# Optimization experiments

Measured on AMD Instinct MI355X. Metric: run time of the kernel, lower is better.

## Reference

```python
import jax, jax.numpy as jnp
import numpy as np

K = 9                # snake kernel size
CENTER = K // 2
EXT = 1.0            # extend_scope
EPS = 1e-5           # GroupNorm eps (torch default)


def conv2d(x, w, b, stride, padding):
    out = jax.lax.conv_general_dilated(
        x, w, window_strides=stride, padding=padding,
        dimension_numbers=("NCHW", "OIHW", "NCHW"))
    return out + b[None, :, None, None]


def group_norm(x, gamma, beta, groups):
    B, C, H, W = x.shape
    xg = x.reshape(B, groups, C // groups, H, W)
    mu = xg.mean(axis=(2, 3, 4), keepdims=True)
    var = xg.var(axis=(2, 3, 4), keepdims=True)
    xn = ((xg - mu) / jnp.sqrt(var + EPS)).reshape(B, C, H, W)
    return xn * gamma[None, :, None, None] + beta[None, :, None, None]


def setup_inputs() -> dict:
    key = jax.random.key(0)
    ks = jax.random.split(key, 6)
    B, Cin, Cout, H, W = 4, 64, 64, 128, 128
    x = jax.random.normal(ks[0], (B, Cin, H, W), jnp.float32)
    w_off = jax.random.normal(ks[1], (2 * K, Cin, 3, 3), jnp.float32) * 0.05
    b_off = jax.random.normal(ks[2], (2 * K,), jnp.float32) * 0.01
    g_gn_off = jnp.ones((2 * K,), jnp.float32)
    b_gn_off = jnp.zeros((2 * K,), jnp.float32)
    w_dsc = jax.random.normal(ks[3], (Cout, Cin, K, 1), jnp.float32) * 0.05
    b_dsc = jax.random.normal(ks[4], (Cout,), jnp.float32) * 0.01
    g_gn = jnp.ones((Cout,), jnp.float32)
    b_gn = jnp.zeros((Cout,), jnp.float32)
    return {"x": x, "w_off": w_off, "b_off": b_off,
            "g_gn_off": g_gn_off, "b_gn_off": b_gn_off,
            "w_dsc": w_dsc, "b_dsc": b_dsc, "g_gn": g_gn, "b_gn": b_gn}


def reference(x, w_off, b_off, g_gn_off, b_gn_off, w_dsc, b_dsc, g_gn, b_gn):
    B, Cin, H, W = x.shape
    # offset branch: conv3x3 -> GN(K groups over 2K chans) -> tanh
    off = conv2d(x, w_off, b_off, (1, 1), "SAME")
    off = jnp.tanh(group_norm(off, g_gn_off, b_gn_off, K))
    y_off = off[:, :K]                              # morph=0 uses y offsets, [B,K,H,W]

    # cumulative offsets outward from the kernel center (center entry = 0)
    upper = jnp.cumsum(y_off[:, CENTER + 1:], axis=1)
    lower = jnp.flip(jnp.cumsum(jnp.flip(y_off[:, :CENTER], axis=1), axis=1), axis=1)
    y_off_new = jnp.concatenate(
        [lower, jnp.zeros_like(y_off[:, :1]), upper], axis=1)   # [B,K,H,W]

    # coordinate maps (pixel space)
    y_coord = jnp.arange(H, dtype=x.dtype)[None, None, :, None] + EXT * y_off_new
    x_spread = jnp.linspace(-CENTER, CENTER, K).astype(x.dtype)
    x_coord = jnp.broadcast_to(
        jnp.arange(W, dtype=x.dtype)[None, None, None, :]
        + x_spread[None, :, None, None], y_coord.shape)
    # rearrange b k h w -> b (h k) w
    y_map = y_coord.transpose(0, 2, 1, 3).reshape(B, H * K, W)
    x_map = x_coord.transpose(0, 2, 1, 3).reshape(B, H * K, W)

    # bilinear grid_sample, align_corners=True; clamp-to-range == torch's
    # _coordinate_map_scaling(clamp + [-1,1] normalize) then grid_sample
    yc = jnp.clip(y_map, 0.0, H - 1.0)
    xc = jnp.clip(x_map, 0.0, W - 1.0)
    y0 = jnp.floor(yc); x0 = jnp.floor(xc)
    wy = yc - y0; wx = xc - x0
    y0i = y0.astype(jnp.int32); x0i = x0.astype(jnp.int32)
    y1i = jnp.minimum(y0i + 1, H - 1); x1i = jnp.minimum(x0i + 1, W - 1)

    def samp(f, y0i, y1i, x0i, x1i, wy, wx):
        # f: [C,H,W]; indices/weights: [K*H, W] -> [C, K*H, W]
        v00 = f[:, y0i, x0i]; v01 = f[:, y0i, x1i]
        v10 = f[:, y1i, x0i]; v11 = f[:, y1i, x1i]
        return (v00 * (1 - wy) * (1 - wx) + v01 * (1 - wy) * wx
                + v10 * wy * (1 - wx) + v11 * wy * wx)

    deformed = jax.vmap(samp)(x, y0i, y1i, x0i, x1i, wy, wx)  # [B,C,K*H,W]

    # snake conv: kernel (K,1), stride (K,1), then GN(out//4) + ReLU
    out = conv2d(deformed, w_dsc, b_dsc, (K, 1), "VALID")      # [B,Cout,H,W]
    out = group_norm(out, g_gn, b_gn, w_dsc.shape[0] // 4)
    return jax.nn.relu(out)
```

## Files before the change

kernel.cpp:

```cpp
#include <hip/hip_runtime.h>
#include <hip/hip_bf16.h>
#include <math.h>

#define B 4
#define C 64
#define H 128
#define W 128
#define KK 9
#define CENTER 4
#define HW (H*W)
#define HP 130
#define WP 130

typedef __attribute__((ext_vector_type(8))) short short8;
typedef __attribute__((ext_vector_type(4))) float f4;

#define OFF_OFFT   0
#define OFF_XB     786432
#define OFF_WB     2949632
#define OFF_WOB    2968064
#define OFF_CSUM   2972672
#define OFF_OSUM   2980864

__device__ __forceinline__ unsigned bf16pack(float a, float b) {
    unsigned ua = __builtin_bit_cast(unsigned, a) + 0x8000u;
    unsigned ub = __builtin_bit_cast(unsigned, b) + 0x8000u;
    return __builtin_amdgcn_perm(ub, ua, 0x07060302);
}

__device__ __forceinline__ unsigned lerp_pack(unsigned a, unsigned b, float fw) {
    float alo = __builtin_bit_cast(float, a << 16);
    float ahi = __builtin_bit_cast(float, a & 0xffff0000u);
    float blo = __builtin_bit_cast(float, b << 16);
    float bhi = __builtin_bit_cast(float, b & 0xffff0000u);
    float slo = alo + fw * (blo - alo);
    float shi = ahi + fw * (bhi - ahi);
    return bf16pack(slo, shi);
}

__device__ __forceinline__ float fast_tanh(float x) {
    float e = __expf(2.f * x);
    return 1.f - 2.f * __builtin_amdgcn_rcpf(e + 1.f);
}

__global__ __launch_bounds__(256) void k_prep(const float* __restrict__ x,
                                              const float* __restrict__ w_dsc,
                                              const float* __restrict__ w_off,
                                              unsigned short* __restrict__ xb,
                                              unsigned short* __restrict__ wb,
                                              unsigned short* __restrict__ wob,
                                              float* __restrict__ csum) {
    int bid = blockIdx.x;
    int tid = threadIdx.x;
    if (bid < 2048) {
        __shared__ float lt[64 * 33];
        int xcd = bid & 7, i = bid >> 3;
        int c = i & 3, hc = (i >> 2) & 15, b = i >> 6;
        int h = (xcd << 4) | hc;
        int w0 = c * 32;
        int ciA = tid >> 2, gA = tid & 3;
        int wlB = tid >> 3, cgB = tid & 7;

        if (c == 0 && tid < 8)
            *(uint4*)(xb + ((size_t)(b * HP + h + 1) * WP) * 64 + tid * 8)
                = make_uint4(0, 0, 0, 0);
        if (c == 3 && tid < 8)
            *(uint4*)(xb + (((size_t)(b * HP + h + 1) * WP) + WP - 1) * 64 + tid * 8)
                = make_uint4(0, 0, 0, 0);
        {
            const float* src = x + ((size_t)(b * C + ciA) * HW) + h * W + w0 + gA * 8;
            float4 v0 = *(const float4*)src;
            float4 v1 = *(const float4*)(src + 4);
            float* d = lt + ciA * 33 + gA * 8;
            d[0] = v0.x; d[1] = v0.y; d[2] = v0.z; d[3] = v0.w;
            d[4] = v1.x; d[5] = v1.y; d[6] = v1.z; d[7] = v1.w;
        }
        __syncthreads();
        {
            unsigned u[4];
#pragma unroll
            for (int i2 = 0; i2 < 4; i2++) {
                float lo = lt[(cgB * 8 + 2 * i2)     * 33 + wlB];
                float hi = lt[(cgB * 8 + 2 * i2 + 1) * 33 + wlB];
                u[i2] = bf16pack(lo, hi);
            }
            *(uint4*)(xb + ((size_t)((b * HP + h + 1) * WP + w0 + wlB + 1)) * 64 + cgB * 8) =
                make_uint4(u[0], u[1], u[2], u[3]);
        }
    } else if (bid < 2048 + 8) {
        int r = bid - 2048;
        int b = r >> 1, which = r & 1;
        unsigned short* dst = xb + ((size_t)(b * HP + which * (HP - 1)) * WP) * 64;
        for (int t = tid; t < WP * 64 / 8; t += 256)
            *(uint4*)(dst + t * 8) = make_uint4(0, 0, 0, 0);
    } else if (bid < 2048 + 8 + 180) {
        int idx = (bid - (2048 + 8)) * 256 + tid;
        if (idx < KK * C * C) {
            int k  = idx >> 12;
            int r  = idx & 4095;
            int co = r >> 6;
            int ci = r & 63;
            unsigned u = __builtin_bit_cast(unsigned, w_dsc[(co * C + ci) * KK + k]);
            u = (u + 0x7fffu + ((u >> 16) & 1u)) >> 16;
            wb[idx] = (unsigned short)u;
        } else if (idx < KK * C * C + 9 * 16 * 64) {
            int r   = idx - KK * C * C;
            int tap = r >> 10;
            int j   = (r >> 6) & 15;
            int ci  = r & 63;
            float v = (j < 10) ? w_off[(j * C + ci) * 9 + tap] : 0.f;
            unsigned u = __builtin_bit_cast(unsigned, v);
            u = (u + 0x7fffu + ((u >> 16) & 1u)) >> 16;
            wob[r] = (unsigned short)u;
        }
    } else {
        int z = bid - (2048 + 8 + 180);
        int base = z * 1024 + tid * 4;
        *(f4*)(csum + base) = 0;
    }
}

__global__ __launch_bounds__(256, 4) void k_offconv(const unsigned short* __restrict__ xb,
                                                    const unsigned short* __restrict__ wob,
                                                    const float* __restrict__ b_off,
                                                    float* __restrict__ offT,
                                                    float* __restrict__ osum16) {
    __shared__ unsigned short wlds[1152 * 8];
    __shared__ float red[80];
    int bid = blockIdx.x;
    int xcd  = bid & 7;
    int i    = bid >> 3;
    int b    = i >> 5;
    int rest = i & 31;
    int h    = (xcd << 4) | (rest >> 1);
    int half = rest & 1;
    int tid  = threadIdx.x;
    int wid  = tid >> 6;
    int lane = tid & 63;
    int lm = lane & 15, qd = lane >> 4;
    int pw = half * 64 + wid * 16;

    for (int c = tid; c < 1152; c += 256) {
        int row = c >> 3, g = c & 7;
        uint4 v = *(const uint4*)(wob + c * 8);
        int dst = (g ^ (row & 7)) * 144 + row;
        *(uint4*)(wlds + dst * 8) = v;
    }
    __syncthreads();

    f4 acc = 0;
    const unsigned short* xrow = xb + ((size_t)(b * HP + h) * WP) * 64;
#pragma unroll
    for (int s = 0; s < 2; s++) {
        int co_ofs = s * 32 + qd * 8;
        short8 a_[9];
#pragma unroll
        for (int t = 0; t < 9; t++) {
            int ky = t / 3, kx = t - 3 * (t / 3);
            a_[t] = *(const short8*)(xrow +
                ((size_t)(ky * WP + pw + lm + kx)) * 64 + co_ofs);
        }
#pragma unroll
        for (int t = 0; t < 9; t++) {
            int row = t * 16 + lm;
            int chunk = (((s * 4 + qd) ^ (lm & 7)) * 144) + row;
            short8 w = *(const short8*)(wlds + chunk * 8);
            acc = __builtin_amdgcn_mfma_f32_16x16x32_bf16(a_[t], w, acc, 0, 0, 0);
        }
    }

    float bo = b_off[lm];
    float sv = 0.f, sq = 0.f;
    int pixbase = (b * H + h) * W;
#pragma unroll
    for (int r = 0; r < 4; r++) {
        float val = acc[r] + bo;
        int p = pw + qd * 4 + r;
        if (lm < 10) {
            offT[(size_t)(pixbase + p) * 12 + lm] = val;
            sv += val; sq += val * val;
        }
    }
    sv += __shfl_xor(sv, 16); sv += __shfl_xor(sv, 32);
    sq += __shfl_xor(sq, 16); sq += __shfl_xor(sq, 32);
    if (lane < 16 && lm < 10) {
        red[(wid * 10 + lm) * 2]     = sv;
        red[(wid * 10 + lm) * 2 + 1] = sq;
    }
    __syncthreads();
    if (tid < 20) {
        int j = tid >> 1, comp = tid & 1;
        float s = red[j * 2 + comp] + red[(10 + j) * 2 + comp] +
                  red[(20 + j) * 2 + comp] + red[(30 + j) * 2 + comp];
        int sidx = (h >> 3) & 15;
        atomicAdd(&osum16[sidx * 40 + b * 10 + (j >> 1) * 2 + comp], s);
    }
}

__global__ __launch_bounds__(256, 4) void k_main(const unsigned short* __restrict__ xb,
                                                 const float* __restrict__ offT,
                                                 const float* __restrict__ osum16,
                                                 const float* __restrict__ g_gn_off,
                                                 const float* __restrict__ b_gn_off,
                                                 const unsigned short* __restrict__ wb,
                                                 const float* __restrict__ b_dsc,
                                                 float* __restrict__ outp,
                                                 float* __restrict__ csum16) {
    __shared__ unsigned short wlds[2304 * 8];
    __shared__ float red[512];
    __shared__ float sred[16];

    int bid = blockIdx.x;
    int xcd  = bid & 7;
    int i    = bid >> 3;
    int b    = i >> 5;
    int rest = i & 31;
    int h    = (xcd << 4) | (rest >> 1);
    int p0   = (rest & 1) << 6;
    int tid  = threadIdx.x;
    int wid  = tid >> 6;
    int lane = tid & 63;
    int lm = lane & 15, qd = lane >> 4;

    int ps = p0 + wid * 16 + lm;

    if (tid < 160) {
        int gc = tid >> 4, s = tid & 15;
        float v = osum16[s * 40 + b * 10 + gc];
        v += __shfl_xor(v, 1); v += __shfl_xor(v, 2);
        v += __shfl_xor(v, 4); v += __shfl_xor(v, 8);
        if (s == 0) sred[gc] = v;
    }
    for (int c = tid; c < 2304; c += 256) {
        int k = c >> 8, row = (c >> 2) & 63, g2 = c & 3;
        uint4 v = *(const uint4*)(wb + (size_t)k * 4096 + row * 64 + g2 * 8);
        int dst = ((g2 ^ (row & 3)) * 576) + k * 64 + row;
        *(uint4*)(wlds + dst * 8) = v;
    }
    __syncthreads();

    float yoff[KK];
    {
        const float inv_n = 1.f / (2.f * HW);
        const float* op = offT + (size_t)((b * H + h) * W + ps) * 12;
        f4 o0 = *(const f4*)op;
        f4 o1 = *(const f4*)(op + 4);
        float o8 = op[8];
        float raw[KK] = {o0[0], o0[1], o0[2], o0[3], o1[0], o1[1], o1[2], o1[3], o8};
        float v[KK];
#pragma unroll
        for (int j = 0; j < KK; j++) {
            int g = j >> 1;
            float s  = sred[g * 2];
            float s2 = sred[g * 2 + 1];
            float mean = s * inv_n;
            float var  = s2 * inv_n - mean * mean;
            float rstd = rsqrtf(var + 1e-5f);
            v[j] = fast_tanh((raw[j] - mean) * rstd * g_gn_off[j] + b_gn_off[j]);
        }
        yoff[CENTER] = 0.f;
        float run = 0.f;
#pragma unroll
        for (int k = CENTER - 1; k >= 0; k--) { run += v[k]; yoff[k] = run; }
        run = 0.f;
#pragma unroll
        for (int k = CENTER + 1; k < KK; k++) { run += v[k]; yoff[k] = run; }
    }

    f4 acc[4];
#pragma unroll
    for (int ct = 0; ct < 4; ct++) acc[ct] = 0;

    auto kpass = [&](int s) {
        int so = s * 32;
#pragma unroll
        for (int kg = 0; kg < 3; kg++) {
            int   ofsA[3], ofsB[3];
            float fw[3];
#pragma unroll
            for (int j = 0; j < 3; j++) {
                int k = kg * 3 + j;
                float yc = fminf(fmaxf((float)h + yoff[k], 0.f), (float)(H - 1));
                float fy = floorf(yc);
                int y0 = (int)fy;
                int dy = (y0 < H - 1) ? (WP * 64) : 0;
                fw[j] = yc - fy;
                int xi = min(max(ps + k - CENTER, 0), W - 1);
                ofsA[j] = ((b * HP + y0 + 1) * WP + xi + 1) * 64 + qd * 8 + so;
                ofsB[j] = ofsA[j] + dy;
            }
            uint4 ga[3], gb[3];
#pragma unroll
            for (int j = 0; j < 3; j++) {
                ga[j] = *(const uint4*)(xb + ofsA[j]);
                gb[j] = *(const uint4*)(xb + ofsB[j]);
            }
#pragma unroll
            for (int j = 0; j < 3; j++) {
                int k = kg * 3 + j;
                uint4 r;
                r.x = lerp_pack(ga[j].x, gb[j].x, fw[j]);
                r.y = lerp_pack(ga[j].y, gb[j].y, fw[j]);
                r.z = lerp_pack(ga[j].z, gb[j].z, fw[j]);
                r.w = lerp_pack(ga[j].w, gb[j].w, fw[j]);
                short8 afr = __builtin_bit_cast(short8, r);
#pragma unroll
                for (int ct = 0; ct < 4; ct++) {
                    int row = ct * 16 + lm;
                    int chunk = ((qd ^ (lm & 3)) * 576) + k * 64 + row;
                    short8 bfr = *(const short8*)(wlds + chunk * 8);
                    acc[ct] = __builtin_amdgcn_mfma_f32_16x16x32_bf16(afr, bfr,
                                                                      acc[ct], 0, 0, 0);
                }
            }
        }
    };

    kpass(0);
    __syncthreads();
    for (int c = tid; c < 2304; c += 256) {
        int k = c >> 8, row = (c >> 2) & 63, g2 = c & 3;
        uint4 v = *(const uint4*)(wb + (size_t)k * 4096 + row * 64 + (4 + g2) * 8);
        int dst = ((g2 ^ (row & 3)) * 576) + k * 64 + row;
        *(uint4*)(wlds + dst * 8) = v;
    }
    __syncthreads();
    kpass(1);

#pragma unroll
    for (int ct = 0; ct < 4; ct++) {
        int co = ct * 16 + lm;
        float bias = b_dsc[co];
        f4 v;
        float sv = 0.f, sq = 0.f;
#pragma unroll
        for (int r = 0; r < 4; r++) {
            v[r] = acc[ct][r] + bias;
            sv += v[r]; sq += v[r] * v[r];
        }
        *(f4*)(outp + ((size_t)(b * C + co)) * HW + h * W + p0 + wid * 16 + qd * 4) = v;
        sv += __shfl_xor(sv, 16); sv += __shfl_xor(sv, 32);
        sq += __shfl_xor(sq, 16); sq += __shfl_xor(sq, 32);
        if (lane < 16) {
            red[((wid * 4 + ct) * 16 + lm) * 2]     = sv;
            red[((wid * 4 + ct) * 16 + lm) * 2 + 1] = sq;
        }
    }
    __syncthreads();
    if (tid < 128) {
        int co = tid >> 1, comp = tid & 1;
        int ct = co >> 4, lmr = co & 15;
        float s = 0.f;
#pragma unroll
        for (int w2 = 0; w2 < 4; w2++)
            s += red[((w2 * 4 + ct) * 16 + lmr) * 2 + comp];
        int sidx = (h >> 3) & 15;
        atomicAdd(&csum16[(sidx * 256 + b * 64 + co) * 2 + comp], s);
    }
}

__global__ __launch_bounds__(256) void k_norm(float* __restrict__ outp,
                                              const float* __restrict__ csum16,
                                              const float* __restrict__ g_gn,
                                              const float* __restrict__ b_gn) {
    __shared__ float lds[128];
    int bid = blockIdx.x;
    int xcd = bid & 7;
    int i   = bid >> 3;
    int bc  = i >> 1;
    int c2  = (xcd << 1) | (i & 1);
    int b = bc >> 6, co = bc & 63;
    int grp = co >> 2;
    int tid = threadIdx.x;

    if (tid < 128) {
        int s = tid >> 3, c = (tid >> 1) & 3, comp = tid & 1;
        lds[tid] = csum16[(s * 256 + b * 64 + grp * 4 + c) * 2 + comp];
    }
    __syncthreads();
#pragma unroll
    for (int st = 64; st >= 2; st >>= 1) {
        if (tid < st) lds[tid] += lds[tid + st];
        __syncthreads();
    }
    float S = lds[0], S2 = lds[1];
    float n = 4.f * HW;
    float mean = S / n;
    float var  = S2 / n - mean * mean;
    float rstd = rsqrtf(var + 1e-5f);
    float sc = rstd * g_gn[co];
    float sh = b_gn[co] - mean * sc;

    int idx = (bc * 16 + c2) * 256 + tid;
    float4* ptr = (float4*)outp;
    float4 vv = ptr[idx];
    vv.x = fmaxf(vv.x * sc + sh, 0.f);
    vv.y = fmaxf(vv.y * sc + sh, 0.f);
    vv.z = fmaxf(vv.z * sc + sh, 0.f);
    vv.w = fmaxf(vv.w * sc + sh, 0.f);
    ptr[idx] = vv;
}

extern "C" void kernel_launch(void* const* d_in, const int* in_sizes, int n_in,
                              void* d_out, int out_size, void* d_ws, size_t ws_size,
                              hipStream_t stream) {
    const float* x        = (const float*)d_in[0];
    const float* w_off    = (const float*)d_in[1];
    const float* b_off    = (const float*)d_in[2];
    const float* g_gn_off = (const float*)d_in[3];
    const float* b_gn_off = (const float*)d_in[4];
    const float* w_dsc    = (const float*)d_in[5];
    const float* b_dsc    = (const float*)d_in[6];
    const float* g_gn     = (const float*)d_in[7];
    const float* b_gn     = (const float*)d_in[8];
    float* out = (float*)d_out;
    float* ws  = (float*)d_ws;

    float*          offT   = ws + OFF_OFFT;
    unsigned short* xbp    = (unsigned short*)(ws + OFF_XB);
    unsigned short* wbp    = (unsigned short*)(ws + OFF_WB);
    unsigned short* wobp   = (unsigned short*)(ws + OFF_WOB);
    float*          csum16 = ws + OFF_CSUM;
    float*          osum16 = ws + OFF_OSUM;

    k_prep<<<2048 + 8 + 180 + 9, 256, 0, stream>>>(x, w_dsc, w_off, xbp, wbp,
                                                   wobp, csum16);
    k_offconv<<<2 * B * H, 256, 0, stream>>>(xbp, wobp, b_off, offT, osum16);
    k_main<<<2 * B * H, 256, 0, stream>>>(xbp, offT, osum16, g_gn_off, b_gn_off,
                                          wbp, b_dsc, out, csum16);
    k_norm<<<B * C * HW / 4 / 256, 256, 0, stream>>>(out, csum16, g_gn, b_gn);
}
```

Measured before the change: 134.9 us.

## Process full row per 512-thread block with whole weight tensor resident in LDS

k_main now uses 512-thread blocks that each cover a full output row of 128 pixels, halving the grid. The whole bf16 snake-conv weight (both channel halves) is staged into LDS once, which removes the mid-kernel barrier and reload between the two channel passes. Gathers for both channel halves are issued together per kernel group to raise memory-level parallelism. The cost is doubled LDS per block (about 74KB), larger blocks, and higher register pressure, all of which can lower occupancy.

New measurement: 137.3 us. About the same (+1.8%).

```diff
diff --git a/kernel.cpp b/kernel.cpp
--- a/kernel.cpp
+++ b/kernel.cpp
@@ -197,7 +197,7 @@
     }
 }
 
-__global__ __launch_bounds__(256, 4) void k_main(const unsigned short* __restrict__ xb,
+__global__ __launch_bounds__(512, 4) void k_main(const unsigned short* __restrict__ xb,
                                                  const float* __restrict__ offT,
                                                  const float* __restrict__ osum16,
                                                  const float* __restrict__ g_gn_off,
@@ -206,23 +206,21 @@
                                                  const float* __restrict__ b_dsc,
                                                  float* __restrict__ outp,
                                                  float* __restrict__ csum16) {
-    __shared__ unsigned short wlds[2304 * 8];
-    __shared__ float red[512];
+    __shared__ unsigned short wlds[4608 * 8];
+    __shared__ float red[1024];
     __shared__ float sred[16];
 
     int bid = blockIdx.x;
     int xcd  = bid & 7;
     int i    = bid >> 3;
-    int b    = i >> 5;
-    int rest = i & 31;
-    int h    = (xcd << 4) | (rest >> 1);
-    int p0   = (rest & 1) << 6;
+    int b    = i >> 4;
+    int h    = (xcd << 4) | (i & 15);
     int tid  = threadIdx.x;
     int wid  = tid >> 6;
     int lane = tid & 63;
     int lm = lane & 15, qd = lane >> 4;
 
-    int ps = p0 + wid * 16 + lm;
+    int ps = wid * 16 + lm;
 
     if (tid < 160) {
         int gc = tid >> 4, s = tid & 15;
@@ -231,10 +229,12 @@
         v += __shfl_xor(v, 4); v += __shfl_xor(v, 8);
         if (s == 0) sred[gc] = v;
     }
-    for (int c = tid; c < 2304; c += 256) {
-        int k = c >> 8, row = (c >> 2) & 63, g2 = c & 3;
-        uint4 v = *(const uint4*)(wb + (size_t)k * 4096 + row * 64 + g2 * 8);
-        int dst = ((g2 ^ (row & 3)) * 576) + k * 64 + row;
+    for (int c = tid; c < 4608; c += 512) {
+        int k = c >> 9, rem = c & 511;
+        int co = rem >> 3, g = rem & 7;
+        int s = g >> 2, g2 = g & 3;
+        uint4 v = *(const uint4*)(wb + (size_t)k * 4096 + co * 64 + g * 8);
+        int dst = s * 2304 + (g2 ^ (co & 3)) * 576 + k * 64 + co;
         *(uint4*)(wlds + dst * 8) = v;
     }
     __syncthreads();
@@ -271,61 +271,51 @@
 #pragma unroll
     for (int ct = 0; ct < 4; ct++) acc[ct] = 0;
 
-    auto kpass = [&](int s) {
-        int so = s * 32;
-#pragma unroll
-        for (int kg = 0; kg < 3; kg++) {
-            int   ofsA[3], ofsB[3];
-            float fw[3];
+#pragma unroll
+    for (int kg = 0; kg < 3; kg++) {
+        int   ofsA[3], ofsB[3];
+        float fw[3];
+#pragma unroll
+        for (int j = 0; j < 3; j++) {
+            int k = kg * 3 + j;
+            float yc = fminf(fmaxf((float)h + yoff[k], 0.f), (float)(H - 1));
+            float fy = floorf(yc);
+            int y0 = (int)fy;
+            int dy = (y0 < H - 1) ? (WP * 64) : 0;
+            fw[j] = yc - fy;
+            int xi = min(max(ps + k - CENTER, 0), W - 1);
+            ofsA[j] = ((b * HP + y0 + 1) * WP + xi + 1) * 64 + qd * 8;
+            ofsB[j] = ofsA[j] + dy;
+        }
+        uint4 ga[2][3], gb[2][3];
+#pragma unroll
+        for (int s = 0; s < 2; s++)
 #pragma unroll
             for (int j = 0; j < 3; j++) {
-                int k = kg * 3 + j;
-                float yc = fminf(fmaxf((float)h + yoff[k], 0.f), (float)(H - 1));
-                float fy = floorf(yc);
-                int y0 = (int)fy;
-                int dy = (y0 < H - 1) ? (WP * 64) : 0;
-                fw[j] = yc - fy;
-                int xi = min(max(ps + k - CENTER, 0), W - 1);
-                ofsA[j] = ((b * HP + y0 + 1) * WP + xi + 1) * 64 + qd * 8 + so;
-                ofsB[j] = ofsA[j] + dy;
+                ga[s][j] = *(const uint4*)(xb + ofsA[j] + s * 32);
+                gb[s][j] = *(const uint4*)(xb + ofsB[j] + s * 32);
             }
-            uint4 ga[3], gb[3];
-#pragma unroll
-            for (int j = 0; j < 3; j++) {
-                ga[j] = *(const uint4*)(xb + ofsA[j]);
-                gb[j] = *(const uint4*)(xb + ofsB[j]);
-            }
+#pragma unroll
+        for (int s = 0; s < 2; s++)
 #pragma unroll
             for (int j = 0; j < 3; j++) {
                 int k = kg * 3 + j;
                 uint4 r;
-                r.x = lerp_pack(ga[j].x, gb[j].x, fw[j]);
-                r.y = lerp_pack(ga[j].y, gb[j].y, fw[j]);
-                r.z = lerp_pack(ga[j].z, gb[j].z, fw[j]);
-                r.w = lerp_pack(ga[j].w, gb[j].w, fw[j]);
+                r.x = lerp_pack(ga[s][j].x, gb[s][j].x, fw[j]);
+                r.y = lerp_pack(ga[s][j].y, gb[s][j].y, fw[j]);
+                r.z = lerp_pack(ga[s][j].z, gb[s][j].z, fw[j]);
+                r.w = lerp_pack(ga[s][j].w, gb[s][j].w, fw[j]);
                 short8 afr = __builtin_bit_cast(short8, r);
 #pragma unroll
                 for (int ct = 0; ct < 4; ct++) {
-                    int row = ct * 16 + lm;
-                    int chunk = ((qd ^ (lm & 3)) * 576) + k * 64 + row;
+                    int co = ct * 16 + lm;
+                    int chunk = s * 2304 + ((qd ^ (lm & 3)) * 576) + k * 64 + co;
                     short8 bfr = *(const short8*)(wlds + chunk * 8);
                     acc[ct] = __builtin_amdgcn_mfma_f32_16x16x32_bf16(afr, bfr,
                                                                       acc[ct], 0, 0, 0);
                 }
             }
-        }
-    };
-
-    kpass(0);
-    __syncthreads();
-    for (int c = tid; c < 2304; c += 256) {
-        int k = c >> 8, row = (c >> 2) & 63, g2 = c & 3;
-        uint4 v = *(const uint4*)(wb + (size_t)k * 4096 + row * 64 + (4 + g2) * 8);
-        int dst = ((g2 ^ (row & 3)) * 576) + k * 64 + row;
-        *(uint4*)(wlds + dst * 8) = v;
-    }
-    __syncthreads();
-    kpass(1);
+    }
 
 #pragma unroll
     for (int ct = 0; ct < 4; ct++) {
@@ -338,7 +328,7 @@
             v[r] = acc[ct][r] + bias;
             sv += v[r]; sq += v[r] * v[r];
         }
-        *(f4*)(outp + ((size_t)(b * C + co)) * HW + h * W + p0 + wid * 16 + qd * 4) = v;
+        *(f4*)(outp + ((size_t)(b * C + co)) * HW + h * W + wid * 16 + qd * 4) = v;
         sv += __shfl_xor(sv, 16); sv += __shfl_xor(sv, 32);
         sq += __shfl_xor(sq, 16); sq += __shfl_xor(sq, 32);
         if (lane < 16) {
@@ -352,7 +342,7 @@
         int ct = co >> 4, lmr = co & 15;
         float s = 0.f;
 #pragma unroll
-        for (int w2 = 0; w2 < 4; w2++)
+        for (int w2 = 0; w2 < 8; w2++)
             s += red[((w2 * 4 + ct) * 16 + lmr) * 2 + comp];
         int sidx = (h >> 3) & 15;
         atomicAdd(&csum16[(sidx * 256 + b * 64 + co) * 2 + comp], s);
@@ -426,7 +416,7 @@
     k_prep<<<2048 + 8 + 180 + 9, 256, 0, stream>>>(x, w_dsc, w_off, xbp, wbp,
                                                    wobp, csum16);
     k_offconv<<<2 * B * H, 256, 0, stream>>>(xbp, wobp, b_off, offT, osum16);
-    k_main<<<2 * B * H, 256, 0, stream>>>(xbp, offT, osum16, g_gn_off, b_gn_off,
-                                          wbp, b_dsc, out, csum16);
+    k_main<<<B * H, 512, 0, stream>>>(xbp, offT, osum16, g_gn_off, b_gn_off,
+                                      wbp, b_dsc, out, csum16);
     k_norm<<<B * C * HW / 4 / 256, 256, 0, stream>>>(out, csum16, g_gn, b_gn);
 }
```
